# Kernel tuning notes

Hardware: AMD Instinct MI355X
Metric: run time of the kernel (lower is better)

The kernel has to match this reference:

```python
import jax, jax.numpy as jnp
import numpy as np

HIDDEN = 1024
NUM_EXPERTS = 8
TOP_K = 2
CAPACITY_FACTOR = 1.5
B, S = 2, 2048


def setup_inputs() -> dict:
    key = jax.random.key(0)
    k0, k1, k2 = jax.random.split(key, 3)
    sc1 = 1.0 / np.sqrt(HIDDEN)
    return {
        "hidden_states": jax.random.normal(k0, (B, S, HIDDEN), dtype=jnp.float32),
        "w1": jax.random.uniform(k1, (HIDDEN, HIDDEN), jnp.float32, -sc1, sc1),
        "b1": jnp.zeros((HIDDEN,), jnp.float32),
        "w2": jax.random.uniform(k2, (NUM_EXPERTS, HIDDEN), jnp.float32, -sc1, sc1),
        "b2": jnp.zeros((NUM_EXPERTS,), jnp.float32),
    }


def reference(hidden_states, w1, b1, w2, b2):
    bsz, seq, hid = hidden_states.shape
    # router MLP: Linear -> ReLU -> Linear
    h = jax.nn.relu(jnp.einsum("bsh,oh->bso", hidden_states, w1) + b1)
    router_logits = jnp.einsum("bsh,eh->bse", h, w2) + b2  # [B,S,E]
    router_probs = jax.nn.softmax(router_logits, axis=-1)

    top_k_probs, top_k_indices = jax.lax.top_k(router_probs, TOP_K)  # [B,S,K]
    top_k_probs = top_k_probs / jnp.sum(top_k_probs, axis=-1, keepdims=True)

    capacity = int(bsz * seq * CAPACITY_FACTOR * TOP_K / NUM_EXPERTS)  # static

    # Original writes ONLY capacity slot 0 for each selected expert.
    onehot = jax.nn.one_hot(top_k_indices, NUM_EXPERTS, dtype=router_probs.dtype)  # [B,S,K,E]
    slot0_dispatch = jnp.sum(onehot, axis=-2)                      # [B,S,E] (top-k experts distinct)
    slot0_combine = jnp.einsum("bske,bsk->bse", onehot, top_k_probs)

    dispatch_tensor = jnp.zeros((bsz, seq, NUM_EXPERTS, capacity), router_probs.dtype)
    dispatch_tensor = dispatch_tensor.at[..., 0].set(slot0_dispatch)
    combine_tensor = jnp.zeros((bsz, seq, NUM_EXPERTS, capacity), router_probs.dtype)
    combine_tensor = combine_tensor.at[..., 0].set(slot0_combine)

    router_prob_per_expert = jnp.mean(router_probs, axis=(0, 1))  # [E]
    aux_loss = jnp.sum(router_prob_per_expert * jnp.log(router_prob_per_expert * NUM_EXPERTS + 1e-9))
    return dispatch_tensor, combine_tensor, router_probs, aux_loss
```

## Files before the change

kernel.cpp:

```cpp
#include <hip/hip_runtime.h>
#include <hip/hip_bf16.h>
#include <math.h>

#define HID  1024
#define NEXP 8
#define CAP  1536
#define NTOK 4096

#define DISP_OFF 0ull
#define COMB_OFF 50331648ull
#define RP_OFF   100663296ull
#define AUX_OFF  100696064ull

typedef float f32x4 __attribute__((ext_vector_type(4)));
typedef short s16x8 __attribute__((ext_vector_type(8)));
typedef unsigned short u16;

#define PART_F 524288
#define OXH_F  526400
#define OXM_F  2623552
#define OWH_F  4720704
#define OWM_F  5244992

__device__ __forceinline__ void cvt8(const float4 v0, const float4 v1, s16x8& hi, s16x8& mi)
{
    float f[8] = {v0.x, v0.y, v0.z, v0.w, v1.x, v1.y, v1.z, v1.w};
#pragma unroll
    for (int i = 0; i < 8; ++i) {
        __hip_bfloat16 h = __float2bfloat16(f[i]);
        float fh = __bfloat162float(h);
        __hip_bfloat16 m = __float2bfloat16(f[i] - fh);
        hi[i] = (short)__builtin_bit_cast(unsigned short, h);
        mi[i] = (short)__builtin_bit_cast(unsigned short, m);
    }
}

__device__ __forceinline__ void gload16(const void* g, void* l)
{
    __builtin_amdgcn_global_load_lds(
        (const __attribute__((address_space(1))) unsigned int*)g,
        (__attribute__((address_space(3))) unsigned int*)l, 16, 0, 0);
}

__global__ __launch_bounds__(256) void zero_kernel(float* __restrict__ out)
{
    f32x4* p = (f32x4*)out + (size_t)blockIdx.x * 12288 + threadIdx.x;
    f32x4 z = (f32x4)0.0f;
#pragma unroll 8
    for (int i = 0; i < 48; ++i) { __builtin_nontemporal_store(z, p); p += 256; }
}

__global__ __launch_bounds__(256) void prep_kernel(
    const float* __restrict__ X, const float* __restrict__ W1, float* __restrict__ ws)
{
    const int g = blockIdx.x * 256 + threadIdx.x;
    const float* src;
    u16 *dh, *dm;
    int idx;
    if (g < 524288) { src = X;  dh = (u16*)(ws + OXH_F); dm = (u16*)(ws + OXM_F); idx = g; }
    else            { src = W1; dh = (u16*)(ws + OWH_F); dm = (u16*)(ws + OWM_F); idx = g - 524288; }
    float4 v0 = *(const float4*)(src + (size_t)idx * 8);
    float4 v1 = *(const float4*)(src + (size_t)idx * 8 + 4);
    s16x8 hi, mi;
    cvt8(v0, v1, hi, mi);
    *(s16x8*)(dh + (size_t)idx * 8) = hi;
    *(s16x8*)(dm + (size_t)idx * 8) = mi;
}

__global__ __launch_bounds__(256) void gemm_kernel(
    const float* __restrict__ B1, const float* __restrict__ W2, float* __restrict__ ws)
{
    __shared__ s16x8 L[2][4][128][8];
    const int tid = threadIdx.x, bid = blockIdx.x;

    const int n0 = (bid & 7) * 128;
    const int m0 = (bid >> 3) * 128;
    const int wave = tid >> 6, lane = tid & 63;
    const int wr = wave >> 1, wc = wave & 1;
    const int fr = lane & 15, fk = lane >> 4;

    const u16* XH = (const u16*)(ws + OXH_F);
    const u16* XM = (const u16*)(ws + OXM_F);
    const u16* WH = (const u16*)(ws + OWH_F);
    const u16* WM = (const u16*)(ws + OWM_F);

    const int sr = lane >> 3, sc = lane & 7;
    const u16* sb = (wave & 2)
        ? (((wave & 1) ? WM : WH) + (size_t)(n0 + sr) * HID + ((sc ^ sr) << 3))
        : (((wave & 1) ? XM : XH) + (size_t)(m0 + sr) * HID + ((sc ^ sr) << 3));
    char* db = (char*)&L[0][wave][0][0];

    f32x4 acc[4][4];
#pragma unroll
    for (int i = 0; i < 4; ++i)
#pragma unroll
        for (int j = 0; j < 4; ++j) acc[i][j] = (f32x4)0.0f;

    {
        const u16* s = sb;
#pragma unroll
        for (int i = 0; i < 16; ++i)
            gload16(s + (size_t)i * 8 * HID, db + i * 1024);
    }
    __syncthreads();

    for (int kk = 0; kk < 16; ++kk) {
        const int b = kk & 1;
        if (kk + 1 < 16) {
            const u16* s = sb + (kk + 1) * 64;
            char* d = db + (b ^ 1) * 65536;
#pragma unroll
            for (int i = 0; i < 16; ++i)
                gload16(s + (size_t)i * 8 * HID, d + i * 1024);
        }

        const s16x8 (*LAh)[8] = L[b][0];
        const s16x8 (*LAm)[8] = L[b][1];
        const s16x8 (*LBh)[8] = L[b][2];
        const s16x8 (*LBm)[8] = L[b][3];
#pragma unroll
        for (int ks = 0; ks < 2; ++ks) {
            const int sl = (ks * 4 + fk) ^ (fr & 7);
            s16x8 bh[4], bm[4];
#pragma unroll
            for (int j = 0; j < 4; ++j) {
                const int rb = wc * 64 + j * 16 + fr;
                bh[j] = LBh[rb][sl];
                bm[j] = LBm[rb][sl];
            }
#pragma unroll
            for (int i = 0; i < 4; ++i) {
                const int ra = wr * 64 + i * 16 + fr;
                s16x8 ah = LAh[ra][sl];
                s16x8 am = LAm[ra][sl];
#pragma unroll
                for (int j = 0; j < 4; ++j) {
                    acc[i][j] = __builtin_amdgcn_mfma_f32_16x16x32_bf16(ah, bh[j], acc[i][j], 0, 0, 0);
                    acc[i][j] = __builtin_amdgcn_mfma_f32_16x16x32_bf16(ah, bm[j], acc[i][j], 0, 0, 0);
                    acc[i][j] = __builtin_amdgcn_mfma_f32_16x16x32_bf16(am, bh[j], acc[i][j], 0, 0, 0);
                }
            }
        }
        __syncthreads();
    }

    const int colbase = n0 + wc * 64 + fr;
#pragma unroll
    for (int j = 0; j < 4; ++j) {
        const float bj = B1[colbase + j * 16];
#pragma unroll
        for (int i = 0; i < 4; ++i)
#pragma unroll
            for (int r = 0; r < 4; ++r)
                acc[i][j][r] = fmaxf(acc[i][j][r] + bj, 0.f);
    }

    const int slice = (bid & 7) * 2 + wc;
    float* pbase = ws + ((size_t)slice * NTOK + (m0 + wr * 64 + fk * 4)) * NEXP;
#pragma unroll
    for (int e = 0; e < 8; ++e) {
        const float w20 = W2[e * HID + colbase];
        const float w21 = W2[e * HID + colbase + 16];
        const float w22 = W2[e * HID + colbase + 32];
        const float w23 = W2[e * HID + colbase + 48];
        float pe[16];
#pragma unroll
        for (int i = 0; i < 4; ++i)
#pragma unroll
            for (int r = 0; r < 4; ++r)
                pe[i * 4 + r] = acc[i][0][r] * w20 + acc[i][1][r] * w21 +
                                acc[i][2][r] * w22 + acc[i][3][r] * w23;
#pragma unroll
        for (int m = 1; m <= 8; m <<= 1)
#pragma unroll
            for (int q = 0; q < 16; ++q)
                pe[q] += __shfl_xor(pe[q], m, 64);
        if (fr == 0) {
#pragma unroll
            for (int i = 0; i < 4; ++i)
#pragma unroll
                for (int r = 0; r < 4; ++r)
                    pbase[(size_t)(i * 16 + r) * NEXP + e] = pe[i * 4 + r];
        }
    }
}

__global__ __launch_bounds__(256) void router2_kernel(
    const float* __restrict__ ws, const float* __restrict__ B2, float* __restrict__ out)
{
    const int t = blockIdx.x * 256 + threadIdx.x;
    float lg[8];
#pragma unroll
    for (int e = 0; e < 8; ++e) lg[e] = 0.f;
#pragma unroll
    for (int s = 0; s < 16; ++s) {
        const float* p = ws + ((size_t)s * NTOK + t) * NEXP;
        f32x4 v0 = *(const f32x4*)p;
        f32x4 v1 = *(const f32x4*)(p + 4);
        lg[0] += v0.x; lg[1] += v0.y; lg[2] += v0.z; lg[3] += v0.w;
        lg[4] += v1.x; lg[5] += v1.y; lg[6] += v1.z; lg[7] += v1.w;
    }
#pragma unroll
    for (int e = 0; e < 8; ++e) lg[e] += B2[e];

    float mx = lg[0];
#pragma unroll
    for (int e = 1; e < 8; ++e) mx = fmaxf(mx, lg[e]);
    float pr[8], s = 0.f;
#pragma unroll
    for (int e = 0; e < 8; ++e) { pr[e] = expf(lg[e] - mx); s += pr[e]; }
    const float inv = 1.f / s;
#pragma unroll
    for (int e = 0; e < 8; ++e) pr[e] *= inv;

    int e1 = 0; float p1 = pr[0];
#pragma unroll
    for (int e = 1; e < 8; ++e) if (pr[e] > p1) { p1 = pr[e]; e1 = e; }
    int e2 = -1; float p2 = -1.f;
#pragma unroll
    for (int e = 0; e < 8; ++e) if (e != e1 && pr[e] > p2) { p2 = pr[e]; e2 = e; }

    const float invs = 1.f / (p1 + p2);
    float* rp = out + RP_OFF + (size_t)t * NEXP;
    f32x4 o0 = {pr[0], pr[1], pr[2], pr[3]};
    f32x4 o1 = {pr[4], pr[5], pr[6], pr[7]};
    *(f32x4*)rp = o0; *(f32x4*)(rp + 4) = o1;

    const size_t base = (size_t)t * NEXP;
    out[DISP_OFF + (base + e1) * CAP] = 1.0f;
    out[DISP_OFF + (base + e2) * CAP] = 1.0f;
    out[COMB_OFF + (base + e1) * CAP] = p1 * invs;
    out[COMB_OFF + (base + e2) * CAP] = p2 * invs;
}

__global__ __launch_bounds__(256) void aux_kernel(float* __restrict__ out)
{
    __shared__ float sm[NEXP][257];
    const int tid = threadIdx.x;
    float s[NEXP];
#pragma unroll
    for (int e = 0; e < 8; ++e) s[e] = 0.f;
    const float* rp = out + RP_OFF;
    for (int t = tid; t < NTOK; t += 256) {
        f32x4 v0 = *(const f32x4*)&rp[(size_t)t * NEXP];
        f32x4 v1 = *(const f32x4*)&rp[(size_t)t * NEXP + 4];
        s[0] += v0.x; s[1] += v0.y; s[2] += v0.z; s[3] += v0.w;
        s[4] += v1.x; s[5] += v1.y; s[6] += v1.z; s[7] += v1.w;
    }
#pragma unroll
    for (int e = 0; e < 8; ++e) sm[e][tid] = s[e];
    __syncthreads();
    for (int st = 128; st > 0; st >>= 1) {
        if (tid < st) {
#pragma unroll
            for (int e = 0; e < 8; ++e) sm[e][tid] += sm[e][tid + st];
        }
        __syncthreads();
    }
    if (tid == 0) {
        float loss = 0.f;
#pragma unroll
        for (int e = 0; e < 8; ++e) {
            float m = sm[e][0] * (1.0f / NTOK);
            loss += m * logf(m * (float)NEXP + 1e-9f);
        }
        out[AUX_OFF] = loss;
    }
}

extern "C" void kernel_launch(void* const* d_in, const int* in_sizes, int n_in,
                              void* d_out, int out_size, void* d_ws, size_t ws_size,
                              hipStream_t stream)
{
    const float* x  = (const float*)d_in[0];
    const float* w1 = (const float*)d_in[1];
    const float* b1 = (const float*)d_in[2];
    const float* w2 = (const float*)d_in[3];
    const float* b2 = (const float*)d_in[4];
    float* out = (float*)d_out;
    float* ws  = (float*)d_ws;

    zero_kernel<<<2048, 256, 0, stream>>>(out);
    prep_kernel<<<2560, 256, 0, stream>>>(x, w1, ws);
    gemm_kernel<<<256, 256, 0, stream>>>(b1, w2, ws);
    router2_kernel<<<16, 256, 0, stream>>>(ws, b2, out);
    aux_kernel<<<1, 256, 0, stream>>>(out);
}
```

Before: 475.2 us.

## Fuse output zeroing into GEMM launch and halve K-tile to cut LDS usage

```diff
diff --git a/kernel.cpp b/kernel.cpp
--- a/kernel.cpp
+++ b/kernel.cpp
@@ -40,14 +40,6 @@
     __builtin_amdgcn_global_load_lds(
         (const __attribute__((address_space(1))) unsigned int*)g,
         (__attribute__((address_space(3))) unsigned int*)l, 16, 0, 0);
-}
-
-__global__ __launch_bounds__(256) void zero_kernel(float* __restrict__ out)
-{
-    f32x4* p = (f32x4*)out + (size_t)blockIdx.x * 12288 + threadIdx.x;
-    f32x4 z = (f32x4)0.0f;
-#pragma unroll 8
-    for (int i = 0; i < 48; ++i) { __builtin_nontemporal_store(z, p); p += 256; }
 }
 
 __global__ __launch_bounds__(256) void prep_kernel(
@@ -67,11 +59,21 @@
     *(s16x8*)(dm + (size_t)idx * 8) = mi;
 }
 
-__global__ __launch_bounds__(256) void gemm_kernel(
-    const float* __restrict__ B1, const float* __restrict__ W2, float* __restrict__ ws)
-{
-    __shared__ s16x8 L[2][4][128][8];
+__global__ void fused_kernel(
+    const float* __restrict__ B1, const float* __restrict__ W2,
+    float* __restrict__ ws, float* __restrict__ out)
+{
+    __shared__ s16x8 L[2][4][128][4];
     const int tid = threadIdx.x, bid = blockIdx.x;
+
+    if (bid >= 256) {
+        const int zid = bid - 256;
+        f32x4* p = (f32x4*)out + (size_t)zid * 98304 + tid;
+        f32x4 z = (f32x4)0.0f;
+#pragma unroll 8
+        for (int i = 0; i < 384; ++i) { __builtin_nontemporal_store(z, p); p += 256; }
+        return;
+    }
 
     const int n0 = (bid & 7) * 128;
     const int m0 = (bid >> 3) * 128;
@@ -84,10 +86,11 @@
     const u16* WH = (const u16*)(ws + OWH_F);
     const u16* WM = (const u16*)(ws + OWM_F);
 
-    const int sr = lane >> 3, sc = lane & 7;
+    const int sr4 = lane >> 2;
+    const int cg  = (lane & 3) ^ (sr4 & 3);
     const u16* sb = (wave & 2)
-        ? (((wave & 1) ? WM : WH) + (size_t)(n0 + sr) * HID + ((sc ^ sr) << 3))
-        : (((wave & 1) ? XM : XH) + (size_t)(m0 + sr) * HID + ((sc ^ sr) << 3));
+        ? (((wave & 1) ? WM : WH) + (size_t)(n0 + sr4) * HID + cg * 8)
+        : (((wave & 1) ? XM : XH) + (size_t)(m0 + sr4) * HID + cg * 8);
     char* db = (char*)&L[0][wave][0][0];
 
     f32x4 acc[4][4];
@@ -96,49 +99,43 @@
 #pragma unroll
         for (int j = 0; j < 4; ++j) acc[i][j] = (f32x4)0.0f;
 
-    {
-        const u16* s = sb;
-#pragma unroll
-        for (int i = 0; i < 16; ++i)
-            gload16(s + (size_t)i * 8 * HID, db + i * 1024);
-    }
+#pragma unroll
+    for (int i = 0; i < 8; ++i)
+        gload16(sb + (size_t)i * 16 * HID, db + i * 1024);
     __syncthreads();
 
-    for (int kk = 0; kk < 16; ++kk) {
+    for (int kk = 0; kk < 32; ++kk) {
         const int b = kk & 1;
-        if (kk + 1 < 16) {
-            const u16* s = sb + (kk + 1) * 64;
-            char* d = db + (b ^ 1) * 65536;
-#pragma unroll
-            for (int i = 0; i < 16; ++i)
-                gload16(s + (size_t)i * 8 * HID, d + i * 1024);
-        }
-
-        const s16x8 (*LAh)[8] = L[b][0];
-        const s16x8 (*LAm)[8] = L[b][1];
-        const s16x8 (*LBh)[8] = L[b][2];
-        const s16x8 (*LBm)[8] = L[b][3];
-#pragma unroll
-        for (int ks = 0; ks < 2; ++ks) {
-            const int sl = (ks * 4 + fk) ^ (fr & 7);
-            s16x8 bh[4], bm[4];
+        if (kk + 1 < 32) {
+            const u16* s = sb + (kk + 1) * 32;
+            char* d = db + (b ^ 1) * 32768;
+#pragma unroll
+            for (int i = 0; i < 8; ++i)
+                gload16(s + (size_t)i * 16 * HID, d + i * 1024);
+        }
+
+        const s16x8 (*LAh)[4] = L[b][0];
+        const s16x8 (*LAm)[4] = L[b][1];
+        const s16x8 (*LBh)[4] = L[b][2];
+        const s16x8 (*LBm)[4] = L[b][3];
+        const int sl = fk ^ (fr & 3);
+        s16x8 bh[4], bm[4];
+#pragma unroll
+        for (int j = 0; j < 4; ++j) {
+            const int rb = wc * 64 + j * 16 + fr;
+            bh[j] = LBh[rb][sl];
+            bm[j] = LBm[rb][sl];
+        }
+#pragma unroll
+        for (int i = 0; i < 4; ++i) {
+            const int ra = wr * 64 + i * 16 + fr;
+            s16x8 ah = LAh[ra][sl];
+            s16x8 am = LAm[ra][sl];
 #pragma unroll
             for (int j = 0; j < 4; ++j) {
-                const int rb = wc * 64 + j * 16 + fr;
-                bh[j] = LBh[rb][sl];
-                bm[j] = LBm[rb][sl];
-            }
-#pragma unroll
-            for (int i = 0; i < 4; ++i) {
-                const int ra = wr * 64 + i * 16 + fr;
-                s16x8 ah = LAh[ra][sl];
-                s16x8 am = LAm[ra][sl];
-#pragma unroll
-                for (int j = 0; j < 4; ++j) {
-                    acc[i][j] = __builtin_amdgcn_mfma_f32_16x16x32_bf16(ah, bh[j], acc[i][j], 0, 0, 0);
-                    acc[i][j] = __builtin_amdgcn_mfma_f32_16x16x32_bf16(ah, bm[j], acc[i][j], 0, 0, 0);
-                    acc[i][j] = __builtin_amdgcn_mfma_f32_16x16x32_bf16(am, bh[j], acc[i][j], 0, 0, 0);
-                }
+                acc[i][j] = __builtin_amdgcn_mfma_f32_16x16x32_bf16(ah, bh[j], acc[i][j], 0, 0, 0);
+                acc[i][j] = __builtin_amdgcn_mfma_f32_16x16x32_bf16(ah, bm[j], acc[i][j], 0, 0, 0);
+                acc[i][j] = __builtin_amdgcn_mfma_f32_16x16x32_bf16(am, bh[j], acc[i][j], 0, 0, 0);
             }
         }
         __syncthreads();
@@ -280,9 +277,8 @@
     float* out = (float*)d_out;
     float* ws  = (float*)d_ws;
 
-    zero_kernel<<<2048, 256, 0, stream>>>(out);
     prep_kernel<<<2560, 256, 0, stream>>>(x, w1, ws);
-    gemm_kernel<<<256, 256, 0, stream>>>(b1, w2, ws);
+    fused_kernel<<<512, 256, 0, stream>>>(b1, w2, ws, out);
     router2_kernel<<<16, 256, 0, stream>>>(ws, b2, out);
     aux_kernel<<<1, 256, 0, stream>>>(out);
 }
```

Result: faster. 442.7 us (-6.8%).
